# Kernel optimization log

Hardware: AMD Instinct MI355X
Metric: run time of the kernel (lower is better)

## Reference

```python
import jax, jax.numpy as jnp
import numpy as np

E, T, H, I, K = 8, 8192, 1024, 4096, 2  # experts, tokens, hidden, intermediate, top_k


def setup_inputs() -> dict:
    key = jax.random.key(0)
    k1, k2, k3, k4 = jax.random.split(key, 4)
    return {
        "hidden_states": jax.random.normal(k1, (T, H), dtype=jnp.float32),
        "router_weight": jax.random.normal(k2, (E, H), dtype=jnp.float32) * 0.02,
        "gate_up_proj": jax.random.normal(k3, (E, 2 * I, H), dtype=jnp.float32) * 0.02,
        "down_proj": jax.random.normal(k4, (E, H, I), dtype=jnp.float32) * 0.02,
    }


def reference(hidden_states, router_weight, gate_up_proj, down_proj):
    x = hidden_states  # [T, H]
    # --- TopKRouter ---
    router_logits = x @ router_weight.T  # [T, E]
    routing_probs = jax.nn.softmax(router_logits.astype(jnp.float32), axis=-1)
    top_k_weights, top_k_indices = jax.lax.top_k(routing_probs, K)  # [T, K]
    top_k_weights = top_k_weights / jnp.sum(top_k_weights, axis=-1, keepdims=True)  # norm_topk_prob
    top_k_weights = top_k_weights.astype(router_logits.dtype)
    # --- MoEExperts: dense combine weight per (token, expert) ---
    # w_dense[t, e] = sum_k top_k_weights[t, k] * (top_k_indices[t, k] == e)
    tok = jnp.arange(x.shape[0])[:, None]
    w_dense = jnp.zeros((x.shape[0], E), dtype=x.dtype).at[tok, top_k_indices].add(top_k_weights)
    out = jnp.zeros_like(x)
    for e in range(E):  # fixed small expert loop (structurally distinct weights)
        gu = x @ gate_up_proj[e].T          # [T, 2I]
        gate, up = jnp.split(gu, 2, axis=-1)
        y = (jax.nn.silu(gate) * up) @ down_proj[e].T  # [T, H]
        out = out + w_dense[:, e:e + 1] * y
    return out
```

## Files before the change

kernel.cpp:

```cpp
#include <hip/hip_runtime.h>
#include <stdint.h>
#include <math.h>

#define NE 8
#define NT 8192
#define NH 1024
#define NI 4096
#define BM 128
#define BK 32

typedef _Float16 half8 __attribute__((ext_vector_type(8)));
typedef float f32x4 __attribute__((ext_vector_type(4)));

#define OFF_X16   (512u << 10)
#define OFF_ACT   (18u << 20)
#define OFF_GUP16 (146ull << 20)
#define OFF_DP16  (274ull << 20)

__device__ __forceinline__ half8 pack_half8v(f32x4 a, f32x4 b) {
  half8 h;
  h[0] = (_Float16)a[0]; h[1] = (_Float16)a[1]; h[2] = (_Float16)a[2]; h[3] = (_Float16)a[3];
  h[4] = (_Float16)b[0]; h[5] = (_Float16)b[1]; h[6] = (_Float16)b[2]; h[7] = (_Float16)b[3];
  return h;
}

__device__ __forceinline__ void gload16(const void* g, void* l) {
  __builtin_amdgcn_global_load_lds(
      (const __attribute__((address_space(1))) uint32_t*)g,
      (__attribute__((address_space(3))) uint32_t*)l, 16, 0, 0);
}

#define PIPE_WAIT(N) asm volatile("s_waitcnt vmcnt(" #N ")" ::: "memory")
#define PIPE_BAR() do { asm volatile("" ::: "memory"); \
                        __builtin_amdgcn_s_barrier(); \
                        asm volatile("" ::: "memory"); } while (0)

__global__ __launch_bounds__(256) void convert_all(
    const float* __restrict__ gup, _Float16* __restrict__ gup16,
    const float* __restrict__ dp,  _Float16* __restrict__ dp16)
{
  const int n8g = NE*2*NI*NH/8;
  const int n8d = NE*NH*NI/8;
  int stride = gridDim.x * 256;
  for (int i = blockIdx.x * 256 + threadIdx.x; i < n8g; i += stride) {
    const f32x4* p = (const f32x4*)(gup + (size_t)i * 8);
    f32x4 a = __builtin_nontemporal_load(p);
    f32x4 b = __builtin_nontemporal_load(p + 1);
    *(half8*)(gup16 + (size_t)i * 8) = pack_half8v(a, b);
  }
  for (int i = blockIdx.x * 256 + threadIdx.x; i < n8d; i += stride) {
    const f32x4* p = (const f32x4*)(dp + (size_t)i * 8);
    f32x4 a = __builtin_nontemporal_load(p);
    f32x4 b = __builtin_nontemporal_load(p + 1);
    *(half8*)(dp16 + (size_t)i * 8) = pack_half8v(a, b);
  }
}

__global__ __launch_bounds__(256) void moe_router(
    const float* __restrict__ x, const float* __restrict__ rw,
    int* __restrict__ iws, _Float16* __restrict__ x16)
{
  int wid  = threadIdx.x >> 6;
  int lane = threadIdx.x & 63;
  int t = (blockIdx.x << 2) + wid;

  const float4* xp4 = (const float4*)(x + (size_t)t * NH + lane * 16);
  float xv[16];
  #pragma unroll
  for (int j = 0; j < 4; ++j) {
    float4 v = xp4[j];
    xv[4*j+0] = v.x; xv[4*j+1] = v.y; xv[4*j+2] = v.z; xv[4*j+3] = v.w;
  }
  half8 h0, h1;
  #pragma unroll
  for (int j = 0; j < 8; ++j) { h0[j] = (_Float16)xv[j]; h1[j] = (_Float16)xv[8+j]; }
  half8* xo = (half8*)(x16 + (size_t)t * NH + lane * 16);
  xo[0] = h0; xo[1] = h1;

  float lg[NE];
  #pragma unroll
  for (int e = 0; e < NE; ++e) {
    const float4* wp4 = (const float4*)(rw + e * NH + lane * 16);
    float s = 0.f;
    #pragma unroll
    for (int j = 0; j < 4; ++j) {
      float4 w = wp4[j];
      s += xv[4*j+0]*w.x + xv[4*j+1]*w.y + xv[4*j+2]*w.z + xv[4*j+3]*w.w;
    }
    lg[e] = s;
  }
  #pragma unroll
  for (int d = 32; d > 0; d >>= 1) {
    #pragma unroll
    for (int e = 0; e < NE; ++e) lg[e] += __shfl_xor(lg[e], d, 64);
  }
  if (lane == 0) {
    int e0 = 0;
    #pragma unroll
    for (int e = 1; e < NE; ++e) if (lg[e] > lg[e0]) e0 = e;
    int e1 = (e0 == 0) ? 1 : 0;
    #pragma unroll
    for (int e = 0; e < NE; ++e) if (e != e0 && lg[e] > lg[e1]) e1 = e;
    float p1 = expf(lg[e1] - lg[e0]);
    float s  = 1.f + p1;
    int*   te = iws + 64;
    float* tw = (float*)(iws + 64 + NT*2);
    te[2*t]   = e0; te[2*t+1] = e1;
    tw[2*t]   = 1.f / s; tw[2*t+1] = p1 / s;
    atomicAdd(iws + e0, 1);
    atomicAdd(iws + e1, 1);
  }
}

__global__ void moe_scan(int* iws) {
  if (threadIdx.x == 0 && blockIdx.x == 0) {
    int* cnt = iws; int* off = iws + 8; int* mbc = iws + 25;
    int o = 0, m = 0;
    for (int e = 0; e < NE; ++e) {
      off[e] = o; mbc[e] = m;
      o += cnt[e];
      m += (cnt[e] + BM - 1) / BM;
    }
    off[NE] = o; mbc[NE] = m;
  }
}

__global__ __launch_bounds__(256) void moe_fill(int* __restrict__ iws) {
  int t = blockIdx.x * 256 + threadIdx.x;
  const int*   te = iws + 64;
  const float* tw = (const float*)(iws + 64 + NT*2);
  int*   cursor   = iws + 17;
  const int* off  = iws + 8;
  int*   tok_slot = iws + 64 + NT*4;
  float* w_slot   = (float*)(iws + 64 + NT*6);
  int*   islot    = iws + 64 + NT*8;
  #pragma unroll
  for (int k = 0; k < 2; ++k) {
    int e = te[2*t+k];
    int pos = atomicAdd(&cursor[e], 1);
    int s = off[e] + pos;
    tok_slot[s] = t;
    w_slot[s]   = tw[2*t+k];
    islot[2*t+k] = s;
  }
}

__global__ __launch_bounds__(256, 2) void moe_gemm1_f16(
    const _Float16* __restrict__ x16, const _Float16* __restrict__ gup16,
    const int* __restrict__ iws, _Float16* __restrict__ act)
{
  const int* cnt = iws; const int* off = iws + 8; const int* mbc = iws + 25;
  const int* tok_slot = iws + 64 + NT*4;
  int bid = blockIdx.x;
  int mb  = bid >> 6;
  int i0  = (bid & 63) << 6;
  if (mb >= mbc[NE]) return;
  int e = 0;
  while (mb >= mbc[e+1]) ++e;
  int mloc  = mb - mbc[e];
  int row0  = off[e] + mloc * BM;
  int nrows = cnt[e] - mloc * BM; if (nrows > BM) nrows = BM;

  __shared__ __align__(16) _Float16 Al [3][BM * BK];
  __shared__ __align__(16) _Float16 Bgl[3][64 * BK];
  __shared__ __align__(16) _Float16 Bul[3][64 * BK];

  int tid = threadIdx.x, wid = tid >> 6, lane = tid & 63;
  int sr0 = wid*16 + (lane >> 2);
  int sr1 = 64 + sr0;
  int slot = lane & 3;
  int ks0 = (slot ^ ((sr0 >> 1) & 3)) * 8;
  int ks1 = (slot ^ ((sr1 >> 1) & 3)) * 8;

  int tok0 = tok_slot[row0 + (sr0 < nrows ? sr0 : 0)];
  int tok1 = tok_slot[row0 + (sr1 < nrows ? sr1 : 0)];
  const _Float16* pA0 = x16 + (size_t)tok0 * NH + ks0;
  const _Float16* pA1 = x16 + (size_t)tok1 * NH + ks1;
  const _Float16* pBg = gup16 + ((size_t)e*2*NI + i0 + sr0) * NH + ks0;
  const _Float16* pBu = pBg + (size_t)NI * NH;

  int wr = (wid >> 1) * 64, wc = (wid & 1) * 32;
  int fr = lane & 15, fq = lane >> 4;

  f32x4 accG[4][2] = {};
  f32x4 accU[4][2] = {};

  _Float16 *A0 = &Al[0][0], *A1 = &Al[1][0], *A2 = &Al[2][0];
  _Float16 *G0 = &Bgl[0][0], *G1 = &Bgl[1][0], *G2 = &Bgl[2][0];
  _Float16 *U0 = &Bul[0][0], *U1 = &Bul[1][0], *U2 = &Bul[2][0];

#define STAGE1(Ab, Gb, Ub, kk) do { \
    gload16(pA0 + (kk), (Ab) + wid*512); \
    gload16(pA1 + (kk), (Ab) + (4+wid)*512); \
    gload16(pBg + (kk), (Gb) + wid*512); \
    gload16(pBu + (kk), (Ub) + wid*512); \
  } while (0)

#define COMPUTE1(Ab, Gb, Ub) do { \
    half8 aF[4]; \
    _Pragma("unroll") \
    for (int m = 0; m < 4; ++m) { \
      int r = wr + m*16 + fr; \
      aF[m] = *(const half8*)((Ab) + r*BK + ((fq ^ ((r>>1)&3)) * 8)); \
    } \
    __builtin_amdgcn_s_setprio(1); \
    _Pragma("unroll") \
    for (int n = 0; n < 2; ++n) { \
      int rb = wc + n*16 + fr; \
      int bo = rb*BK + ((fq ^ ((rb>>1)&3)) * 8); \
      half8 bg = *(const half8*)((Gb) + bo); \
      half8 bu = *(const half8*)((Ub) + bo); \
      _Pragma("unroll") \
      for (int m = 0; m < 4; ++m) \
        accG[m][n] = __builtin_amdgcn_mfma_f32_16x16x32_f16(aF[m], bg, accG[m][n], 0, 0, 0); \
      _Pragma("unroll") \
      for (int m = 0; m < 4; ++m) \
        accU[m][n] = __builtin_amdgcn_mfma_f32_16x16x32_f16(aF[m], bu, accU[m][n], 0, 0, 0); \
    } \
    __builtin_amdgcn_s_setprio(0); \
  } while (0)

#define ROT1() do { _Float16* t_; \
    t_ = A0; A0 = A1; A1 = A2; A2 = t_; \
    t_ = G0; G0 = G1; G1 = G2; G2 = t_; \
    t_ = U0; U0 = U1; U1 = U2; U2 = t_; } while (0)

  STAGE1(A0, G0, U0, 0);
  STAGE1(A1, G1, U1, BK);

  for (int k0 = 0; k0 + 2*BK < NH; k0 += BK) {
    PIPE_WAIT(4);
    PIPE_BAR();
    STAGE1(A2, G2, U2, k0 + 2*BK);
    COMPUTE1(A0, G0, U0);
    ROT1();
  }
  PIPE_WAIT(4);
  PIPE_BAR();
  COMPUTE1(A0, G0, U0);
  ROT1();
  PIPE_WAIT(0);
  PIPE_BAR();
  COMPUTE1(A0, G0, U0);

#undef STAGE1
#undef COMPUTE1
#undef ROT1

  #pragma unroll
  for (int m = 0; m < 4; ++m) {
    #pragma unroll
    for (int j = 0; j < 4; ++j) {
      int rl = wr + m*16 + fq*4 + j;
      if (rl < nrows) {
        _Float16* dst = act + (size_t)(row0 + rl) * NI + i0 + wc + fr;
        #pragma unroll
        for (int n = 0; n < 2; ++n) {
          float g = accG[m][n][j], u = accU[m][n][j];
          float a = (g / (1.f + __expf(-g))) * u;
          dst[n*16] = (_Float16)a;
        }
      }
    }
  }
}

__global__ __launch_bounds__(256, 2) void moe_gemm2_f16(
    const _Float16* __restrict__ act, const _Float16* __restrict__ dp16,
    const int* __restrict__ iws, float* __restrict__ y)
{
  const int* cnt = iws; const int* off = iws + 8; const int* mbc = iws + 25;
  const float* w_slot = (const float*)(iws + 64 + NT*6);
  int bid = blockIdx.x;
  int mb  = ((bid >> 6) << 3) | (bid & 7);
  int h0  = ((bid >> 3) & 7) << 7;
  if (mb >= mbc[NE]) return;
  int e = 0;
  while (mb >= mbc[e+1]) ++e;
  int mloc  = mb - mbc[e];
  int row0  = off[e] + mloc * BM;
  int nrows = cnt[e] - mloc * BM; if (nrows > BM) nrows = BM;

  __shared__ __align__(16) _Float16 Al[3][BM  * BK];
  __shared__ __align__(16) _Float16 Bl[3][128 * BK];

  int tid = threadIdx.x, wid = tid >> 6, lane = tid & 63;
  int sr0 = wid*16 + (lane >> 2);
  int sr1 = 64 + sr0;
  int slot = lane & 3;
  int ks0 = (slot ^ ((sr0 >> 1) & 3)) * 8;
  int ks1 = (slot ^ ((sr1 >> 1) & 3)) * 8;

  const _Float16* pA0 = act + (size_t)(row0 + (sr0 < nrows ? sr0 : 0)) * NI + ks0;
  const _Float16* pA1 = act + (size_t)(row0 + (sr1 < nrows ? sr1 : 0)) * NI + ks1;
  const _Float16* pB0 = dp16 + ((size_t)e*NH + h0 + sr0) * NI + ks0;
  const _Float16* pB1 = dp16 + ((size_t)e*NH + h0 + sr1) * NI + ks1;

  int wr = (wid >> 1) * 64, wc = (wid & 1) * 64;
  int fr = lane & 15, fq = lane >> 4;

  f32x4 acc[4][4] = {};

  _Float16 *A0 = &Al[0][0], *A1 = &Al[1][0], *A2 = &Al[2][0];
  _Float16 *B0 = &Bl[0][0], *B1 = &Bl[1][0], *B2 = &Bl[2][0];

#define STAGE2(Ab, Bb, kk) do { \
    gload16(pA0 + (kk), (Ab) + wid*512); \
    gload16(pA1 + (kk), (Ab) + (4+wid)*512); \
    gload16(pB0 + (kk), (Bb) + wid*512); \
    gload16(pB1 + (kk), (Bb) + (4+wid)*512); \
  } while (0)

#define COMPUTE2(Ab, Bb) do { \
    half8 aF[4]; \
    _Pragma("unroll") \
    for (int m = 0; m < 4; ++m) { \
      int r = wr + m*16 + fr; \
      aF[m] = *(const half8*)((Ab) + r*BK + ((fq ^ ((r>>1)&3)) * 8)); \
    } \
    __builtin_amdgcn_s_setprio(1); \
    _Pragma("unroll") \
    for (int n = 0; n < 4; ++n) { \
      int rb = wc + n*16 + fr; \
      half8 b = *(const half8*)((Bb) + rb*BK + ((fq ^ ((rb>>1)&3)) * 8)); \
      _Pragma("unroll") \
      for (int m = 0; m < 4; ++m) \
        acc[m][n] = __builtin_amdgcn_mfma_f32_16x16x32_f16(aF[m], b, acc[m][n], 0, 0, 0); \
    } \
    __builtin_amdgcn_s_setprio(0); \
  } while (0)

#define ROT2() do { _Float16* t_; \
    t_ = A0; A0 = A1; A1 = A2; A2 = t_; \
    t_ = B0; B0 = B1; B1 = B2; B2 = t_; } while (0)

  STAGE2(A0, B0, 0);
  STAGE2(A1, B1, BK);

  for (int k0 = 0; k0 + 2*BK < NI; k0 += BK) {
    PIPE_WAIT(4);
    PIPE_BAR();
    STAGE2(A2, B2, k0 + 2*BK);
    COMPUTE2(A0, B0);
    ROT2();
  }
  PIPE_WAIT(4);
  PIPE_BAR();
  COMPUTE2(A0, B0);
  ROT2();
  PIPE_WAIT(0);
  PIPE_BAR();
  COMPUTE2(A0, B0);

#undef STAGE2
#undef COMPUTE2
#undef ROT2

  #pragma unroll
  for (int m = 0; m < 4; ++m) {
    #pragma unroll
    for (int j = 0; j < 4; ++j) {
      int rl = wr + m*16 + fq*4 + j;
      if (rl < nrows) {
        int slotr = row0 + rl;
        float wgt = w_slot[slotr];
        float* dst = y + (size_t)slotr * NH + h0 + wc + fr;
        #pragma unroll
        for (int n = 0; n < 4; ++n)
          dst[n*16] = acc[m][n][j] * wgt;
      }
    }
  }
}

__global__ __launch_bounds__(256) void moe_combine(
    const float* __restrict__ y, const int* __restrict__ iws,
    float* __restrict__ out)
{
  const int* islot = iws + 64 + NT*8;
  int t = blockIdx.x;
  int s0 = islot[2*t], s1 = islot[2*t+1];
  const f32x4* y0 = (const f32x4*)(y + (size_t)s0 * NH);
  const f32x4* y1 = (const f32x4*)(y + (size_t)s1 * NH);
  f32x4* o = (f32x4*)(out + (size_t)t * NH);
  int i = threadIdx.x;
  o[i] = y0[i] + y1[i];
}

extern "C" void kernel_launch(void* const* d_in, const int* in_sizes, int n_in,
                              void* d_out, int out_size, void* d_ws, size_t ws_size,
                              hipStream_t stream) {
  const float* x   = (const float*)d_in[0];
  const float* rw  = (const float*)d_in[1];
  const float* gup = (const float*)d_in[2];
  const float* dp  = (const float*)d_in[3];
  float* out = (float*)d_out;
  int* iws = (int*)d_ws;
  _Float16* x16   = (_Float16*)((char*)d_ws + OFF_X16);
  _Float16* act   = (_Float16*)((char*)d_ws + OFF_ACT);
  _Float16* gup16 = (_Float16*)((char*)d_ws + OFF_GUP16);
  _Float16* dp16  = (_Float16*)((char*)d_ws + OFF_DP16);
  float* y = (float*)((char*)d_ws + OFF_GUP16);

  hipMemsetAsync(d_ws, 0, 512, stream);

  convert_all<<<4096, 256, 0, stream>>>(gup, gup16, dp, dp16);

  moe_router<<<NT / 4, 256, 0, stream>>>(x, rw, iws, x16);
  moe_scan<<<1, 64, 0, stream>>>(iws);
  moe_fill<<<NT / 256, 256, 0, stream>>>(iws);

  int nmb = NT * 2 / BM + NE;
  moe_gemm1_f16<<<nmb * (NI / 64), 256, 0, stream>>>(x16, gup16, iws, act);
  moe_gemm2_f16<<<nmb * (NH / 128), 256, 0, stream>>>(act, dp16, iws, y);
  moe_combine<<<NT, 256, 0, stream>>>(y, iws, out);
}
```

Baseline: 968.4 us.

## Fuse weight conversion into router and gemm1 kernels to overlap with compute

Converting gate_up weights to fp16 now happens in extra blocks of the router kernel, and converting down_proj weights happens in every ninth block of the gemm1 kernel. The standalone conversion pass is gone. The aim is to hide bandwidth-bound conversion behind router and GEMM compute and to cut one launch. In exchange, block-index remapping makes the schedule more complex, and conversion blocks compete with GEMM blocks for bandwidth and CU slots.

```diff
diff --git a/kernel.cpp b/kernel.cpp
--- a/kernel.cpp
+++ b/kernel.cpp
@@ -35,34 +35,27 @@
                         __builtin_amdgcn_s_barrier(); \
                         asm volatile("" ::: "memory"); } while (0)
 
-__global__ __launch_bounds__(256) void convert_all(
-    const float* __restrict__ gup, _Float16* __restrict__ gup16,
-    const float* __restrict__ dp,  _Float16* __restrict__ dp16)
+__global__ __launch_bounds__(256) void conv_router(
+    const float* __restrict__ x, const float* __restrict__ rw,
+    int* __restrict__ iws, _Float16* __restrict__ x16,
+    const float* __restrict__ gup, _Float16* __restrict__ gup16)
 {
-  const int n8g = NE*2*NI*NH/8;
-  const int n8d = NE*NH*NI/8;
-  int stride = gridDim.x * 256;
-  for (int i = blockIdx.x * 256 + threadIdx.x; i < n8g; i += stride) {
-    const f32x4* p = (const f32x4*)(gup + (size_t)i * 8);
-    f32x4 a = __builtin_nontemporal_load(p);
-    f32x4 b = __builtin_nontemporal_load(p + 1);
-    *(half8*)(gup16 + (size_t)i * 8) = pack_half8v(a, b);
-  }
-  for (int i = blockIdx.x * 256 + threadIdx.x; i < n8d; i += stride) {
-    const f32x4* p = (const f32x4*)(dp + (size_t)i * 8);
-    f32x4 a = __builtin_nontemporal_load(p);
-    f32x4 b = __builtin_nontemporal_load(p + 1);
-    *(half8*)(dp16 + (size_t)i * 8) = pack_half8v(a, b);
-  }
-}
-
-__global__ __launch_bounds__(256) void moe_router(
-    const float* __restrict__ x, const float* __restrict__ rw,
-    int* __restrict__ iws, _Float16* __restrict__ x16)
-{
+  int bid = blockIdx.x;
+  if (bid >= 2048) {
+    int cbid = bid - 2048;
+    const int n8g = NE*2*NI*NH/8;
+    int stride = 4096 * 256;
+    for (int i = cbid * 256 + threadIdx.x; i < n8g; i += stride) {
+      const f32x4* p = (const f32x4*)(gup + (size_t)i * 8);
+      f32x4 a = __builtin_nontemporal_load(p);
+      f32x4 b = __builtin_nontemporal_load(p + 1);
+      *(half8*)(gup16 + (size_t)i * 8) = pack_half8v(a, b);
+    }
+    return;
+  }
   int wid  = threadIdx.x >> 6;
   int lane = threadIdx.x & 63;
-  int t = (blockIdx.x << 2) + wid;
+  int t = (bid << 2) + wid;
 
   const float4* xp4 = (const float4*)(x + (size_t)t * NH + lane * 16);
   float xv[16];
@@ -147,11 +140,26 @@
 
 __global__ __launch_bounds__(256, 2) void moe_gemm1_f16(
     const _Float16* __restrict__ x16, const _Float16* __restrict__ gup16,
-    const int* __restrict__ iws, _Float16* __restrict__ act)
+    const int* __restrict__ iws, _Float16* __restrict__ act,
+    const float* __restrict__ dp, _Float16* __restrict__ dp16)
 {
+  int bidr = blockIdx.x;
+  int grp = bidr / 9, rem = bidr - grp * 9;
+  if (rem == 8) {
+    const int n8d = NE*NH*NI/8;
+    int stride = 1088 * 256;
+    for (int i = grp * 256 + threadIdx.x; i < n8d; i += stride) {
+      const f32x4* p = (const f32x4*)(dp + (size_t)i * 8);
+      f32x4 a = __builtin_nontemporal_load(p);
+      f32x4 b = __builtin_nontemporal_load(p + 1);
+      *(half8*)(dp16 + (size_t)i * 8) = pack_half8v(a, b);
+    }
+    return;
+  }
+  int bid = grp * 8 + rem;
+
   const int* cnt = iws; const int* off = iws + 8; const int* mbc = iws + 25;
   const int* tok_slot = iws + 64 + NT*4;
-  int bid = blockIdx.x;
   int mb  = bid >> 6;
   int i0  = (bid & 63) << 6;
   if (mb >= mbc[NE]) return;
@@ -404,14 +412,11 @@
 
   hipMemsetAsync(d_ws, 0, 512, stream);
 
-  convert_all<<<4096, 256, 0, stream>>>(gup, gup16, dp, dp16);
-
-  moe_router<<<NT / 4, 256, 0, stream>>>(x, rw, iws, x16);
+  conv_router<<<6144, 256, 0, stream>>>(x, rw, iws, x16, gup, gup16);
   moe_scan<<<1, 64, 0, stream>>>(iws);
   moe_fill<<<NT / 256, 256, 0, stream>>>(iws);
 
-  int nmb = NT * 2 / BM + NE;
-  moe_gemm1_f16<<<nmb * (NI / 64), 256, 0, stream>>>(x16, gup16, iws, act);
-  moe_gemm2_f16<<<nmb * (NH / 128), 256, 0, stream>>>(act, dp16, iws, y);
+  moe_gemm1_f16<<<9792, 256, 0, stream>>>(x16, gup16, iws, act, dp, dp16);
+  moe_gemm2_f16<<<(NT * 2 / BM + NE) * (NH / 128), 256, 0, stream>>>(act, dp16, iws, y);
   moe_combine<<<NT, 256, 0, stream>>>(y, iws, out);
 }
```

Measured after the change: 920.1 us. 1.05x faster.
